# Optimization experiments

Hardware: AMD Instinct MI355X
Metric: run time of the kernel (lower is better)

## Reference

```python
import jax, jax.numpy as jnp
import numpy as np

SCALE = 10  # scaling_factor
ETA = 1.0   # init arg eta
EPS = 1e-20


def setup_inputs() -> dict:
    key = jax.random.key(0)
    k1, k2, k3 = jax.random.split(key, 3)
    B, H, W = 32, 1280, 1280
    h, w = H // SCALE, W // SCALE
    output = jax.random.uniform(k1, (B, 1, H, W), dtype=jnp.float32)
    target = jax.random.uniform(k2, (B, 1, H, W), dtype=jnp.float32)
    inp = jax.random.uniform(k3, (B, 1, h, w), dtype=jnp.float32)
    return {"output": output, "target": target, "inp": inp}


def _box_downsample(x):
    # scipy valid convolve2d with ones(10,10)/100 then [::10,::10] strided slice
    # == non-overlapping 10x10 average pooling (H, W divisible by 10).
    B, H, W = x.shape
    return x.reshape(B, H // SCALE, SCALE, W // SCALE, SCALE).mean(axis=(2, 4))


def reference(output, target, inp):
    # MSE term: conv output is computed from detached numpy in the original,
    # so no gradient flows through the pooling path -> stop_gradient.
    pooled = jax.lax.stop_gradient(_box_downsample(output[:, 0]))  # [B, h, w]
    mse = jnp.mean(ETA * (inp[:, 0] - pooled) ** 2)
    # BCE-style term with exact-zero replacement (matches x[x==0]=1e-20)
    om = jnp.where(output == 0, EPS, output)
    oc_raw = 1.0 - output
    oc = jnp.where(oc_raw == 0, EPS, oc_raw)
    bce = -jnp.mean(target * jnp.log(om) + (1.0 - target) * jnp.log(oc))
    loss = mse + bce
    return jnp.full((1, 1), loss)  # original returns a (1,1) tensor
```

## Files before the change

kernel.cpp:

```cpp
#include <hip/hip_runtime.h>


#define BATCH 32
#define HH 1280
#define WW 1280
#define PH 128
#define PW 128
#define SC 10
#define NT 320
#define KD 10
#define NB (BATCH * PH)
#define NT2 512

static constexpr float EPSV = 1e-20f;
static constexpr float LN2  = 0.6931471805599453f;
static constexpr float INV_NBCE = 1.0f / (float)(BATCH * HH * WW);
static constexpr float INV_NM   = 1.0f / (float)(BATCH * PH * PW);

__global__ __launch_bounds__(NT, 4) void srloss_partial(
    const float* __restrict__ output,
    const float* __restrict__ target,
    const float* __restrict__ inp,
    float* __restrict__ partials)
{
    __shared__ float psum[PW];
    __shared__ float red[NT / 64];

    const int t = threadIdx.x;
    const int band = blockIdx.x;
    const int b = band >> 7;
    const int pr = band & 127;

    if (t < PW) psum[t] = 0.0f;
    __syncthreads();

    const size_t base = ((size_t)b * HH + (size_t)pr * SC) * WW;
    const float4* __restrict__ o4p = (const float4*)(output + base) + t;
    const float4* __restrict__ t4p = (const float4*)(target + base) + t;

    float4 ob[KD], tb[KD];
    #pragma unroll
    for (int k = 0; k < KD; ++k) {
        ob[k] = o4p[NT * k];
        tb[k] = t4p[NT * k];
    }

    float acc2 = 0.0f;
    float accd = 0.0f;
    float s0 = 0.0f, s1 = 0.0f;
    #pragma unroll
    for (int k = 0; k < KD; ++k) {
        const float o[4]  = {ob[k].x, ob[k].y, ob[k].z, ob[k].w};
        const float tg[4] = {tb[k].x, tb[k].y, tb[k].z, tb[k].w};
        #pragma unroll
        for (int j = 0; j < 4; ++j) {
            const float om = fmaxf(o[j], EPSV);
            const float oc = fmaxf(1.0f - o[j], EPSV);
            const float l1 = __log2f(om);
            const float l2 = __log2f(oc);
            acc2 += l2;
            accd += tg[j] * (l1 - l2);
        }
        s0 += o[0] + o[1];
        s1 += o[2] + o[3];
    }
    const float bce_acc = LN2 * (acc2 + accd);

    const int col0 = 4 * t;
    const int p0 = col0 / SC;
    if ((col0 % SC) == 8) {
        atomicAdd(&psum[p0],     s0);
        atomicAdd(&psum[p0 + 1], s1);
    } else {
        atomicAdd(&psum[p0], s0 + s1);
    }
    __syncthreads();

    float mse_acc = 0.0f;
    if (t < PW) {
        const float pooled = psum[t] * (1.0f / (float)(SC * SC));
        const float iv = inp[(size_t)band * PW + t];
        const float d = iv - pooled;
        mse_acc = d * d;
    }

    float contrib = (-INV_NBCE) * bce_acc + INV_NM * mse_acc;

    #pragma unroll
    for (int off = 32; off > 0; off >>= 1)
        contrib += __shfl_down(contrib, off, 64);
    if ((t & 63) == 0) red[t >> 6] = contrib;
    __syncthreads();

    if (t == 0) {
        float s = 0.0f;
        #pragma unroll
        for (int w = 0; w < NT / 64; ++w) s += red[w];
        partials[band] = s;
    }
}

__global__ __launch_bounds__(NT2) void srloss_reduce(
    const float* __restrict__ partials,
    float* __restrict__ out)
{
    __shared__ float red[NT2 / 64];
    const int t = threadIdx.x;

    const float4 v0 = ((const float4*)partials)[t];
    const float4 v1 = ((const float4*)partials)[t + NT2];
    float s = (v0.x + v0.y) + (v0.z + v0.w) + (v1.x + v1.y) + (v1.z + v1.w);

    #pragma unroll
    for (int off = 32; off > 0; off >>= 1)
        s += __shfl_down(s, off, 64);
    if ((t & 63) == 0) red[t >> 6] = s;
    __syncthreads();
    if (t == 0) {
        float tot = 0.0f;
        #pragma unroll
        for (int w = 0; w < NT2 / 64; ++w) tot += red[w];
        out[0] = tot;
    }
}

extern "C" void kernel_launch(void* const* d_in, const int* in_sizes, int n_in,
                              void* d_out, int out_size, void* d_ws, size_t ws_size,
                              hipStream_t stream) {
    const float* output = (const float*)d_in[0];
    const float* target = (const float*)d_in[1];
    const float* inp    = (const float*)d_in[2];
    float* out = (float*)d_out;
    float* partials = (float*)d_ws;

    srloss_partial<<<NB, NT, 0, stream>>>(output, target, inp, partials);
    srloss_reduce<<<1, NT2, 0, stream>>>(partials, out);
}
```

Measured before the change: 407.2 us.

## Stage input rows through LDS via direct global-to-LDS loads in two chunks

Replaces the direct register loads of all ten rows with `global_load_lds` asynchronous copies that stage five rows of output and target at a time into shared memory, then read them back as float4. The aim is to cut register pressure and let the hardware DMA path feed LDS. The cost is 51 KB of LDS per block, which limits blocks per CU. There are also extra barriers, and the chunks are serialized with no overlap between loading and compute.

```diff
diff --git a/kernel.cpp b/kernel.cpp
--- a/kernel.cpp
+++ b/kernel.cpp
@@ -8,7 +8,8 @@
 #define PW 128
 #define SC 10
 #define NT 320
-#define KD 10
+#define RPC 5
+#define NCH 2
 #define NB (BATCH * PH)
 #define NT2 512
 
@@ -17,12 +18,19 @@
 static constexpr float INV_NBCE = 1.0f / (float)(BATCH * HH * WW);
 static constexpr float INV_NM   = 1.0f / (float)(BATCH * PH * PW);
 
+#define STAGE16(gp, lp)                                                   \
+    __builtin_amdgcn_global_load_lds(                                     \
+        (const __attribute__((address_space(1))) void*)(const void*)(gp), \
+        (__attribute__((address_space(3))) void*)(void*)(lp), 16, 0, 0)
+
 __global__ __launch_bounds__(NT, 4) void srloss_partial(
     const float* __restrict__ output,
     const float* __restrict__ target,
     const float* __restrict__ inp,
     float* __restrict__ partials)
 {
+    __shared__ float so[RPC * WW];
+    __shared__ float st[RPC * WW];
     __shared__ float psum[PW];
     __shared__ float red[NT / 64];
 
@@ -32,43 +40,55 @@
     const int pr = band & 127;
 
     if (t < PW) psum[t] = 0.0f;
-    __syncthreads();
 
     const size_t base = ((size_t)b * HH + (size_t)pr * SC) * WW;
-    const float4* __restrict__ o4p = (const float4*)(output + base) + t;
-    const float4* __restrict__ t4p = (const float4*)(target + base) + t;
+    const float* op = output + base + 4 * t;
+    const float* tp = target + base + 4 * t;
 
-    float4 ob[KD], tb[KD];
-    #pragma unroll
-    for (int k = 0; k < KD; ++k) {
-        ob[k] = o4p[NT * k];
-        tb[k] = t4p[NT * k];
-    }
+    const int wbase = (t >> 6) << 8;
+
+    const int col0 = 4 * t;
+    const int p0 = col0 / SC;
+    const bool straddle = (col0 % SC) == 8;
 
     float acc2 = 0.0f;
     float accd = 0.0f;
     float s0 = 0.0f, s1 = 0.0f;
+
     #pragma unroll
-    for (int k = 0; k < KD; ++k) {
-        const float o[4]  = {ob[k].x, ob[k].y, ob[k].z, ob[k].w};
-        const float tg[4] = {tb[k].x, tb[k].y, tb[k].z, tb[k].w};
+    for (int h = 0; h < NCH; ++h) {
+        __syncthreads();
+
         #pragma unroll
-        for (int j = 0; j < 4; ++j) {
-            const float om = fmaxf(o[j], EPSV);
-            const float oc = fmaxf(1.0f - o[j], EPSV);
-            const float l1 = __log2f(om);
-            const float l2 = __log2f(oc);
-            acc2 += l2;
-            accd += tg[j] * (l1 - l2);
+        for (int r = 0; r < RPC; ++r) {
+            const int row = h * RPC + r;
+            STAGE16(op + (size_t)row * WW, &so[r * WW + wbase]);
+            STAGE16(tp + (size_t)row * WW, &st[r * WW + wbase]);
         }
-        s0 += o[0] + o[1];
-        s1 += o[2] + o[3];
+        __syncthreads();
+
+        #pragma unroll
+        for (int r = 0; r < RPC; ++r) {
+            const float4 o4 = *(const float4*)&so[r * WW + 4 * t];
+            const float4 t4 = *(const float4*)&st[r * WW + 4 * t];
+            const float o[4]  = {o4.x, o4.y, o4.z, o4.w};
+            const float tg[4] = {t4.x, t4.y, t4.z, t4.w};
+            #pragma unroll
+            for (int j = 0; j < 4; ++j) {
+                const float om = fmaxf(o[j], EPSV);
+                const float oc = fmaxf(1.0f - o[j], EPSV);
+                const float l1 = __log2f(om);
+                const float l2 = __log2f(oc);
+                acc2 += l2;
+                accd += tg[j] * (l1 - l2);
+            }
+            s0 += o[0] + o[1];
+            s1 += o[2] + o[3];
+        }
     }
     const float bce_acc = LN2 * (acc2 + accd);
 
-    const int col0 = 4 * t;
-    const int p0 = col0 / SC;
-    if ((col0 % SC) == 8) {
+    if (straddle) {
         atomicAdd(&psum[p0],     s0);
         atomicAdd(&psum[p0 + 1], s1);
     } else {
```

After: 407.1 us. About the same (-0.0%).
